# Kernel tuning notes

Measured on AMD Instinct MI355X. Metric: run time of the kernel, lower is better.

## Reference

```python
import jax, jax.numpy as jnp
import numpy as np

K_PERIODS = 4   # k_periods
PMAX = 64       # pmax
MIN_P = 16      # min_period_threshold (already clamped to <= PMAX)


def setup_inputs() -> dict:
    key = jax.random.key(0)
    B, T, N = 32, 512, 128
    x = jax.random.normal(key, (B, T, N), dtype=jnp.float32)
    return {"x": x}


def reference(x):
    # x: [B, T, N]
    B, T, N = x.shape
    K = K_PERIODS
    seqs = jnp.transpose(x, (0, 2, 1)).reshape(B * N, T)  # [BN, T]

    # top-k nonzero frequencies by rFFT amplitude
    spec = jnp.fft.rfft(seqs, axis=-1)                    # [BN, T//2+1]
    amp = jnp.abs(spec)
    amp = amp.at[..., 0].set(0.0)                         # zero DC component
    kamp, kidx = jax.lax.top_k(amp, K)                    # [BN, K] each
    kidx = jnp.maximum(kidx, 1)

    # periods and cycle counts
    P = jnp.clip(T // kidx, MIN_P, PMAX)                  # [BN, K]
    cycles = jnp.maximum(T // P, 1)                       # [BN, K]
    take = cycles * P

    # static upper bound on cycles (torch uses data-dependent cycles.max();
    # extra trailing cycle slots here are fully masked to zero)
    Cmax = T // MIN_P
    idx_c = jnp.arange(Cmax)                              # [Cmax]
    idx_p = jnp.arange(PMAX)                              # [Pmax]

    base = jnp.maximum(T - take, 0)[..., None, None]      # [BN, K, 1, 1]
    indices = base + idx_c[None, None, :, None] * P[..., None, None] \
              + idx_p[None, None, None, :]                # [BN, K, Cmax, Pmax]
    indices = jnp.clip(indices, 0, T - 1)

    # gather: broadcast seqs over (K, Cmax)
    gathered = jnp.take_along_axis(seqs[:, None, None, :], indices, axis=-1)

    mask = ((idx_c[None, None, :, None] < cycles[..., None, None]) &
            (idx_p[None, None, None, :] < P[..., None, None])).astype(x.dtype)
    gathered = gathered * mask

    gathered = gathered.reshape(B, N, K, Cmax, PMAX)
    mask = mask.reshape(B, N, K, Cmax, PMAX)
    kamp = kamp.reshape(B, N, K)
    return gathered, mask, kamp
```

## Files before the change

### kernel.cpp

```cpp
#include <hip/hip_runtime.h>
#include <math.h>

#define TLEN 512
#define NCH  128
#define KP   4
#define PMAXV 64
#define CMAXV 32
#define MINP 16
#define NSEQ 4096
#define OUTG ((size_t)NSEQ * KP * CMAXV * PMAXV)

__global__ __launch_bounds__(256) void periodicity_kernel(
    const float* __restrict__ x,
    float* __restrict__ out_g,
    float* __restrict__ out_m,
    float* __restrict__ out_a)
{
    const int s   = blockIdx.x;
    const int tid = threadIdx.x;

    __shared__ float   seqf[TLEN];
    __shared__ double2 X[TLEN];
    __shared__ double2 W[TLEN / 2];
    __shared__ double  amp[TLEN / 2 + 1];
    __shared__ double  rv[256];
    __shared__ int     ri[256];
    __shared__ double  bestv[KP];
    __shared__ int     besti[KP];
    __shared__ int     Ps[KP], Cs[KP], Bs[KP];

    const int b = s >> 7;
    const int n = s & (NCH - 1);
    const float* col = x + (size_t)b * TLEN * NCH + n;
    for (int i = tid; i < TLEN; i += 256)
        seqf[i] = col[(size_t)i * NCH];

    {
        double ang = -6.283185307179586476925286766559 * (double)tid / (double)TLEN;
        double sv, cv;
        sincos(ang, &sv, &cv);
        W[tid] = make_double2(cv, sv);
    }
    __syncthreads();

    for (int i = tid; i < TLEN; i += 256) {
        int r = (int)(__brev((unsigned)i) >> 23);
        X[i] = make_double2((double)seqf[r], 0.0);
    }
    __syncthreads();

    for (int st = 1; st <= 9; ++st) {
        const int half = 1 << (st - 1);
        const int pos  = tid & (half - 1);
        const int i1   = ((tid >> (st - 1)) << st) + pos;
        const int i2   = i1 + half;
        const double2 wv = W[pos << (9 - st)];
        const double2 a  = X[i1];
        const double2 c  = X[i2];
        const double tr = wv.x * c.x - wv.y * c.y;
        const double ti = wv.x * c.y + wv.y * c.x;
        X[i1] = make_double2(a.x + tr, a.y + ti);
        X[i2] = make_double2(a.x - tr, a.y - ti);
        __syncthreads();
    }

    {
        double2 v = X[tid];
        amp[tid] = (tid == 0) ? 0.0 : sqrt(v.x * v.x + v.y * v.y);
        if (tid == 0) {
            double2 vn = X[TLEN / 2];
            amp[TLEN / 2] = sqrt(vn.x * vn.x + vn.y * vn.y);
        }
    }
    __syncthreads();

    for (int q = 0; q < KP; ++q) {
        double v = amp[tid];
        int    idx = tid;
        if (tid == 0) {
            double v2 = amp[TLEN / 2];
            if (v2 > v) { v = v2; idx = TLEN / 2; }
        }
        rv[tid] = v; ri[tid] = idx;
        __syncthreads();
        for (int off = 128; off > 0; off >>= 1) {
            if (tid < off) {
                double ov = rv[tid + off];
                int    oi = ri[tid + off];
                if (ov > rv[tid] || (ov == rv[tid] && oi < ri[tid])) {
                    rv[tid] = ov; ri[tid] = oi;
                }
            }
            __syncthreads();
        }
        if (tid == 0) {
            bestv[q] = rv[0];
            besti[q] = ri[0];
            amp[ri[0]] = -1.0;
        }
        __syncthreads();
    }

    if (tid < KP) {
        int ki = besti[tid];
        if (ki < 1) ki = 1;
        int P = TLEN / ki;
        P = P < MINP ? MINP : (P > PMAXV ? PMAXV : P);
        int cyc = TLEN / P;
        Ps[tid] = P;
        Cs[tid] = cyc;
        Bs[tid] = TLEN - cyc * P;
        out_a[(size_t)s * KP + tid] = (float)bestv[tid];
    }
    __syncthreads();

    float* og = out_g + (size_t)s * (KP * CMAXV * PMAXV);
    float* om = out_m + (size_t)s * (KP * CMAXV * PMAXV);
    const int pp = (tid & 15) << 2;
    for (int r = tid >> 4; r < KP * CMAXV; r += 16) {
        const int k = r >> 5;
        const int c = r & (CMAXV - 1);
        const int P = Ps[k], cyc = Cs[k], base = Bs[k];
        float4 g = make_float4(0.f, 0.f, 0.f, 0.f);
        float4 m = make_float4(0.f, 0.f, 0.f, 0.f);
        if (c < cyc) {
            const int idx = base + c * P + pp;
            if (pp     < P) { g.x = seqf[idx];     m.x = 1.f; }
            if (pp + 1 < P) { g.y = seqf[idx + 1]; m.y = 1.f; }
            if (pp + 2 < P) { g.z = seqf[idx + 2]; m.z = 1.f; }
            if (pp + 3 < P) { g.w = seqf[idx + 3]; m.w = 1.f; }
        }
        *(float4*)(og + r * PMAXV + pp) = g;
        *(float4*)(om + r * PMAXV + pp) = m;
    }
}

extern "C" void kernel_launch(void* const* d_in, const int* in_sizes, int n_in,
                              void* d_out, int out_size, void* d_ws, size_t ws_size,
                              hipStream_t stream) {
    const float* x = (const float*)d_in[0];
    float* out = (float*)d_out;
    float* og = out;
    float* om = out + OUTG;
    float* oa = om + OUTG;
    periodicity_kernel<<<dim3(NSEQ), dim3(256), 0, stream>>>(x, og, om, oa);
}
```

Baseline: 281.6 us.

## Replace block barriers with wave-local sync in FFT and top-k selection

The first seven FFT stages and the bit-reversal load now use wave barriers in place of block-wide __syncthreads, because each 64-lane wave works on its own 128-element chunk until stage 8. The top-k search now runs in one wave using register shuffles instead of a shared-memory tree reduction with many block barriers. This cuts synchronisation overhead in a kernel that is mostly bound by output writes. The risk is that it depends on wave-local data independence and on 64-wide waves.

New measurement: 277.4 us. About the same (-1.5%).

```diff
diff --git a/kernel.cpp b/kernel.cpp
--- a/kernel.cpp
+++ b/kernel.cpp
@@ -16,15 +16,15 @@
     float* __restrict__ out_m,
     float* __restrict__ out_a)
 {
-    const int s   = blockIdx.x;
-    const int tid = threadIdx.x;
+    const int s    = blockIdx.x;
+    const int tid  = threadIdx.x;
+    const int lane = tid & 63;
+    const int wave = tid >> 6;
 
     __shared__ float   seqf[TLEN];
     __shared__ double2 X[TLEN];
     __shared__ double2 W[TLEN / 2];
     __shared__ double  amp[TLEN / 2 + 1];
-    __shared__ double  rv[256];
-    __shared__ int     ri[256];
     __shared__ double  bestv[KP];
     __shared__ int     besti[KP];
     __shared__ int     Ps[KP], Cs[KP], Bs[KP];
@@ -34,7 +34,6 @@
     const float* col = x + (size_t)b * TLEN * NCH + n;
     for (int i = tid; i < TLEN; i += 256)
         seqf[i] = col[(size_t)i * NCH];
-
     {
         double ang = -6.283185307179586476925286766559 * (double)tid / (double)TLEN;
         double sv, cv;
@@ -43,13 +42,18 @@
     }
     __syncthreads();
 
-    for (int i = tid; i < TLEN; i += 256) {
-        int r = (int)(__brev((unsigned)i) >> 23);
-        X[i] = make_double2((double)seqf[r], 0.0);
+    {
+        const int base = wave << 7;
+        int i0 = base + lane, i1 = base + 64 + lane;
+        int r0 = (int)(__brev((unsigned)i0) >> 23);
+        int r1 = (int)(__brev((unsigned)i1) >> 23);
+        X[i0] = make_double2((double)seqf[r0], 0.0);
+        X[i1] = make_double2((double)seqf[r1], 0.0);
     }
-    __syncthreads();
+    __builtin_amdgcn_wave_barrier();
 
-    for (int st = 1; st <= 9; ++st) {
+    #pragma unroll
+    for (int st = 1; st <= 7; ++st) {
         const int half = 1 << (st - 1);
         const int pos  = tid & (half - 1);
         const int i1   = ((tid >> (st - 1)) << st) + pos;
@@ -61,8 +65,25 @@
         const double ti = wv.x * c.y + wv.y * c.x;
         X[i1] = make_double2(a.x + tr, a.y + ti);
         X[i2] = make_double2(a.x - tr, a.y - ti);
+        __builtin_amdgcn_wave_barrier();
+    }
+
+    #pragma unroll
+    for (int st = 8; st <= 9; ++st) {
         __syncthreads();
+        const int half = 1 << (st - 1);
+        const int pos  = tid & (half - 1);
+        const int i1   = ((tid >> (st - 1)) << st) + pos;
+        const int i2   = i1 + half;
+        const double2 wv = W[pos << (9 - st)];
+        const double2 a  = X[i1];
+        const double2 c  = X[i2];
+        const double tr = wv.x * c.x - wv.y * c.y;
+        const double ti = wv.x * c.y + wv.y * c.x;
+        X[i1] = make_double2(a.x + tr, a.y + ti);
+        X[i2] = make_double2(a.x - tr, a.y - ti);
     }
+    __syncthreads();
 
     {
         double2 v = X[tid];
@@ -74,43 +95,43 @@
     }
     __syncthreads();
 
-    for (int q = 0; q < KP; ++q) {
-        double v = amp[tid];
-        int    idx = tid;
-        if (tid == 0) {
-            double v2 = amp[TLEN / 2];
-            if (v2 > v) { v = v2; idx = TLEN / 2; }
+    if (wave == 0) {
+        for (int q = 0; q < KP; ++q) {
+            double v  = amp[lane];
+            int    vi = lane;
+            #pragma unroll
+            for (int j = 1; j < 4; ++j) {
+                double u = amp[lane + 64 * j];
+                if (u > v) { v = u; vi = lane + 64 * j; }
+            }
+            if (lane == 0) {
+                double u = amp[256];
+                if (u > v) { v = u; vi = 256; }
+            }
+            #pragma unroll
+            for (int off = 32; off > 0; off >>= 1) {
+                double ov = __shfl_xor(v, off, 64);
+                int    oi = __shfl_xor(vi, off, 64);
+                if (ov > v || (ov == v && oi < vi)) { v = ov; vi = oi; }
+            }
+            if (lane == 0) {
+                bestv[q] = v;
+                besti[q] = vi;
+                amp[vi] = -1.0;
+            }
+            __builtin_amdgcn_wave_barrier();
         }
-        rv[tid] = v; ri[tid] = idx;
-        __syncthreads();
-        for (int off = 128; off > 0; off >>= 1) {
-            if (tid < off) {
-                double ov = rv[tid + off];
-                int    oi = ri[tid + off];
-                if (ov > rv[tid] || (ov == rv[tid] && oi < ri[tid])) {
-                    rv[tid] = ov; ri[tid] = oi;
-                }
-            }
-            __syncthreads();
+        if (lane < KP) {
+            int ki = besti[lane];
+            if (ki < 1) ki = 1;
+            int P = TLEN / ki;
+            P = P < MINP ? MINP : (P > PMAXV ? PMAXV : P);
+            int cyc = TLEN / P;
+            Ps[lane] = P;
+            Cs[lane] = cyc;
+            Bs[lane] = TLEN - cyc * P;
+            out_a[(size_t)s * KP + lane] = (float)bestv[lane];
         }
-        if (tid == 0) {
-            bestv[q] = rv[0];
-            besti[q] = ri[0];
-            amp[ri[0]] = -1.0;
-        }
-        __syncthreads();
-    }
-
-    if (tid < KP) {
-        int ki = besti[tid];
-        if (ki < 1) ki = 1;
-        int P = TLEN / ki;
-        P = P < MINP ? MINP : (P > PMAXV ? PMAXV : P);
-        int cyc = TLEN / P;
-        Ps[tid] = P;
-        Cs[tid] = cyc;
-        Bs[tid] = TLEN - cyc * P;
-        out_a[(size_t)s * KP + tid] = (float)bestv[tid];
     }
     __syncthreads();
 
```
